# Kernel tuning notes

Measured on AMD Instinct MI355X. Metric: run time of the kernel, lower is better.

The kernel has to match this reference:

```python
import jax, jax.numpy as jnp
import numpy as np

B, N, DIM, H, DH, M = 4, 8192, 1024, 16, 64, 128
SCALE = DH ** -0.5


def setup_inputs() -> dict:
    key = jax.random.key(0)
    ks = jax.random.split(key, 8)
    x = jax.random.normal(ks[0], (B, N, DIM), jnp.float32)
    mask = jnp.ones((B, N), dtype=bool)
    W_qkv = jax.random.normal(ks[1], (DIM, 3 * H * DH), jnp.float32) * 0.02
    agent_tokens = jax.random.normal(ks[2], (H, M, DH), jnp.float32) * 0.02
    W_qa = jax.random.normal(ks[3], (H, H), jnp.float32) * 0.25
    W_ak = jax.random.normal(ks[4], (H, H), jnp.float32) * 0.25
    W_gate = jax.random.normal(ks[5], (DIM, H), jnp.float32) * 0.02
    b_gate = jnp.zeros((H,), jnp.float32)
    W_out = jax.random.normal(ks[6], (H * DH, DIM), jnp.float32) * 0.02
    return {"x": x, "mask": mask, "W_qkv": W_qkv, "agent_tokens": agent_tokens,
            "W_qa": W_qa, "W_ak": W_ak, "W_gate": W_gate, "b_gate": b_gate,
            "W_out": W_out}


def reference(x, mask, W_qkv, agent_tokens, W_qa, W_ak, W_gate, b_gate, W_out):
    b, n, dim = x.shape
    h, m, dh = agent_tokens.shape
    # qkv projection: 'b n (qkv h d) -> qkv b h n d'
    qkv = (x @ W_qkv).reshape(b, n, 3, h, dh).transpose(2, 0, 3, 1, 4)
    q, k, v = qkv[0], qkv[1], qkv[2]  # each [b,h,n,dh]
    a = agent_tokens * (dh ** -0.5)   # [h,m,dh]
    # two-hop similarities
    qa_sim = jnp.einsum('bhid,hjd->bhij', q, a)   # [b,h,n,m]
    ak_sim = jnp.einsum('hid,bhjd->bhij', a, k)   # [b,h,m,n]
    neg = -jnp.finfo(ak_sim.dtype).max
    ak_sim = jnp.where(mask[:, None, None, :], ak_sim, neg)
    qa_attn = jax.nn.softmax(qa_sim, axis=-1)
    ak_attn = jax.nn.softmax(ak_sim, axis=-1)
    # talking heads: 1x1 conv over head dim
    qa_attn = jnp.einsum('xh,bhij->bxij', W_qa, qa_attn)
    ak_attn = jnp.einsum('xh,bhij->bxij', W_ak, ak_attn)
    agent_gathered = jnp.einsum('bhmj,bhjd->bhmd', ak_attn, v)   # [b,h,m,dh]
    out = jnp.einsum('bhim,bhmd->bhid', qa_attn, agent_gathered)  # [b,h,n,dh]
    out = jnp.where(mask[:, None, :, None], out, 0.0)
    # sigmoid gate: 'b n h -> b h n 1'
    gates = jax.nn.sigmoid(jnp.einsum('bnd,dh->bnh', x, W_gate) + b_gate)
    out = out * gates.transpose(0, 2, 1)[..., None]
    # 'b h n d -> b n (h d)' then out projection
    out = out.transpose(0, 2, 1, 3).reshape(b, n, h * dh) @ W_out
    return out
```

## Files before the change

### kernel.cpp

```cpp
#include <hip/hip_runtime.h>

typedef __bf16 bf16_t;
typedef __bf16 bf16x8 __attribute__((ext_vector_type(8)));
typedef __bf16 bf16x4 __attribute__((ext_vector_type(4)));
typedef float  f32x4  __attribute__((ext_vector_type(4)));

#define B_    4
#define N_    8192
#define DIM_  1024
#define H_    16
#define DH_   64
#define M_    128
#define NT_   (B_*N_)
#define NQKV_ 3328

#define MFMA(a,b,c) __builtin_amdgcn_mfma_f32_16x16x32_bf16(a,b,c,0,0,0)

static __device__ __forceinline__ void gld_lds16(const bf16_t* g, char* l) {
  __builtin_amdgcn_global_load_lds(
      (const __attribute__((address_space(1))) unsigned int*)g,
      (__attribute__((address_space(3))) unsigned int*)l, 16, 0, 0);
}

__global__ void k_cvt(const float* __restrict__ in, bf16_t* __restrict__ out,
                      long n8) {
  long i = (long)blockIdx.x * blockDim.x + threadIdx.x;
  if (i >= n8) return;
  const float4* in4 = (const float4*)in;
  float4 f0 = in4[2*i], f1 = in4[2*i+1];
  bf16x8 o;
  o[0]=(__bf16)f0.x; o[1]=(__bf16)f0.y; o[2]=(__bf16)f0.z; o[3]=(__bf16)f0.w;
  o[4]=(__bf16)f1.x; o[5]=(__bf16)f1.y; o[6]=(__bf16)f1.z; o[7]=(__bf16)f1.w;
  ((bf16x8*)out)[i] = o;
}

__device__ __forceinline__ void tcvt_tile(const float* __restrict__ in,
                                          bf16_t* __restrict__ out,
                                          int R, int C, int bx, int by,
                                          bf16_t (*t)[33]) {
  int c0 = bx*32, r0 = by*32;
  int j = threadIdx.x & 31, i8 = threadIdx.x >> 5;
  for (int p = 0; p < 4; ++p) {
    int i = i8 + p*8, r = r0 + i, c = c0 + j;
    if (r < R && c < C) t[i][j] = (__bf16)in[(long)r*C + c];
  }
  __syncthreads();
  for (int p = 0; p < 4; ++p) {
    int i = i8 + p*8, c = c0 + i, r = r0 + j;
    if (c < C && r < R) out[(long)c*R + r] = t[j][i];
  }
}

__global__ void k_prep(const float* __restrict__ Wqkv, const float* __restrict__ Wgate,
                       const float* __restrict__ Wout, const float* __restrict__ agent,
                       bf16_t* __restrict__ WqkvT, bf16_t* __restrict__ WoutT,
                       bf16_t* __restrict__ a_s) {
  __shared__ __align__(16) bf16_t t[32][33];
  int bid = blockIdx.x;
  if (bid < 3072) {
    tcvt_tile(Wqkv, WqkvT, 1024, 3072, bid % 96, bid / 96, t);
  } else if (bid < 3104) {
    tcvt_tile(Wgate, WqkvT + (size_t)3072*DIM_, 1024, 16, 0, bid - 3072, t);
  } else if (bid < 4128) {
    int r = bid - 3104;
    tcvt_tile(Wout, WoutT, 1024, 1024, r % 32, r / 32, t);
  } else if (bid < 4192) {
    long i = (long)(bid - 4128) * 256 + threadIdx.x;
    const float4* in4 = (const float4*)agent;
    float4 f0 = in4[2*i], f1 = in4[2*i+1];
    bf16x8 o;
    o[0]=(__bf16)(f0.x*0.125f); o[1]=(__bf16)(f0.y*0.125f);
    o[2]=(__bf16)(f0.z*0.125f); o[3]=(__bf16)(f0.w*0.125f);
    o[4]=(__bf16)(f1.x*0.125f); o[5]=(__bf16)(f1.y*0.125f);
    o[6]=(__bf16)(f1.z*0.125f); o[7]=(__bf16)(f1.w*0.125f);
    ((bf16x8*)a_s)[i] = o;
  } else {
    long i = (long)(bid - 4192) * 256 + threadIdx.x;
    ((bf16x8*)(WqkvT + (size_t)3200*DIM_))[i] = (bf16x8){};
  }
}

template<int MODE>
__global__ __launch_bounds__(512, 2)
void k_g256(const bf16_t* __restrict__ A, const bf16_t* __restrict__ Bt,
            void* __restrict__ Cout, bf16_t* __restrict__ k2out,
            bf16_t* __restrict__ vTout,
            const float* __restrict__ bg, float* __restrict__ gates,
            int Ndim, int Kdim) {
  __shared__ __align__(16) char lds[131072];
  const int tid = threadIdx.x;
  const int wid = tid >> 6, lane = tid & 63;
  const int g = lane >> 4, r15 = lane & 15;
  const int wr = wid >> 2, wc = wid & 3;
  const int nbx = gridDim.x;
  const int flat = blockIdx.y * nbx + blockIdx.x;
  const int q8 = (nbx * gridDim.y) >> 3;
  const int swz = (flat & 7) * q8 + (flat >> 3);
  const long m0 = (long)(swz / nbx) * 256, n0 = (long)(swz % nbx) * 256;

  f32x4 acc[8][4] = {};
  const int ITERS = Kdim >> 7;

  auto stg = [&](const bf16_t* Gp, long grow0, int tile, int ab, int half) {
    char* base = lds + (((tile & 1)*2 + ab)*2 + half)*16384;
    long kb = (long)tile * 64;
    #pragma unroll
    for (int j = 0; j < 2; ++j) {
      int o = tid*16 + j*8192;
      int row = o >> 7;
      int c16 = ((o >> 4) & 7) ^ (row & 7);
      const bf16_t* src = Gp + (grow0 + half*128 + row)*Kdim + kb + c16*8;
      gld_lds16(src, base + (tid & ~63)*16 + j*8192);
    }
  };
  auto aread = [&](int buf, int q, bf16x8 af[2][2]) {
    const char* base = lds + ((buf*2 + 0)*2 + wr)*16384;
    #pragma unroll
    for (int ml = 0; ml < 2; ++ml) {
      int rl = q*32 + ml*16 + r15;
      #pragma unroll
      for (int kk = 0; kk < 2; ++kk)
        af[ml][kk] = *(const bf16x8*)(base + rl*128 + ((kk*64 + g*16) ^ ((rl & 7) << 4)));
    }
  };
  auto bread = [&](int buf, bf16x8 bf[4][2]) {
    const char* base = lds + ((buf*2 + 1)*2 + (wc >> 1))*16384;
    #pragma unroll
    for (int ni = 0; ni < 4; ++ni) {
      int rl = (wc & 1)*64 + ni*16 + r15;
      #pragma unroll
      for (int kk = 0; kk < 2; ++kk)
        bf[ni][kk] = *(const bf16x8*)(base + rl*128 + ((kk*64 + g*16) ^ ((rl & 7) << 4)));
    }
  };

  stg(A, m0, 0, 0, 0); stg(A, m0, 0, 0, 1);
  stg(Bt, n0, 0, 1, 0); stg(Bt, n0, 0, 1, 1);
  stg(Bt, n0, 1, 1, 0); stg(Bt, n0, 1, 1, 1);

  for (int it = 0; it < ITERS; ++it) {
    const int t0 = 2*it, t1 = 2*it + 1;
    const bool more = (it < ITERS - 1);
    bf16x8 bf[4][2], af[2][2];

#define PH_MFMA(q)                                                        \
    __builtin_amdgcn_s_setprio(1);                                        \
    _Pragma("unroll")                                                     \
    for (int ml = 0; ml < 2; ++ml)                                        \
      _Pragma("unroll")                                                   \
      for (int ni = 0; ni < 4; ++ni)                                      \
        _Pragma("unroll")                                                 \
        for (int kk = 0; kk < 2; ++kk)                                    \
          acc[(q)*2+ml][ni] = MFMA(af[ml][kk], bf[ni][kk], acc[(q)*2+ml][ni]); \
    __builtin_amdgcn_s_setprio(0);
#define BAR asm volatile("s_barrier" ::: "memory")

    stg(A, m0, t1, 0, 0);
    asm volatile("s_waitcnt vmcnt(4)" ::: "memory");
    BAR;
    bread(0, bf); aread(0, 0, af);
    PH_MFMA(0); BAR;
    aread(0, 1, af);
    stg(A, m0, t1, 0, 1);
    BAR; PH_MFMA(1); BAR;
    aread(0, 2, af);
    if (more) stg(Bt, n0, t0 + 2, 1, 0);
    BAR; PH_MFMA(2); BAR;
    aread(0, 3, af);
    if (more) stg(Bt, n0, t0 + 2, 1, 1);
    BAR; PH_MFMA(3); BAR;
    if (more) {
      stg(A, m0, t0 + 2, 0, 0);
      asm volatile("s_waitcnt vmcnt(4)" ::: "memory");
    } else {
      asm volatile("s_waitcnt vmcnt(0)" ::: "memory");
    }
    BAR;
    bread(1, bf); aread(1, 0, af);
    PH_MFMA(0); BAR;
    aread(1, 1, af);
    if (more) stg(A, m0, t0 + 2, 0, 1);
    BAR; PH_MFMA(1); BAR;
    aread(1, 2, af);
    if (more) stg(Bt, n0, t1 + 2, 1, 0);
    BAR; PH_MFMA(2); BAR;
    aread(1, 3, af);
    if (more) stg(Bt, n0, t1 + 2, 1, 1);
    BAR; PH_MFMA(3); BAR;
#undef PH_MFMA
#undef BAR
  }

  if (MODE == 1 && n0 >= 3072) {
    if (wc == 0) {
      float bgv = bg[r15];
      #pragma unroll
      for (int mi = 0; mi < 8; ++mi)
        #pragma unroll
        for (int r = 0; r < 4; ++r) {
          long tok = m0 + wr*128 + mi*16 + g*4 + r;
          float v = acc[mi][0][r] + bgv;
          gates[tok*16 + r15] = 1.0f / (1.0f + __expf(-v));
        }
    }
  } else if (MODE == 1 && n0 >= 2048) {
    long bidx = m0 >> 13;
    long nbase = (m0 & (N_-1)) + wr*128 + g*4;
    #pragma unroll
    for (int mi = 0; mi < 8; ++mi)
      #pragma unroll
      for (int ni = 0; ni < 4; ++ni) {
        long c = (n0 - 2048) + wc*64 + ni*16 + r15;
        bf16x4 o;
        #pragma unroll
        for (int r = 0; r < 4; ++r) o[r] = (__bf16)acc[mi][ni][r];
        *(bf16x4*)(vTout + (bidx*DIM_ + c)*N_ + nbase + mi*16) = o;
      }
  } else if (MODE == 1 && n0 >= 1024) {
    int h = (int)((n0 - 1024 + wc*64) >> 6);
    #pragma unroll
    for (int mi = 0; mi < 8; ++mi)
      #pragma unroll
      for (int ni = 0; ni < 4; ++ni) {
        int dh = ni*16 + r15;
        #pragma unroll
        for (int r = 0; r < 4; ++r) {
          long row = m0 + wr*128 + mi*16 + g*4 + r;
          long bidx = row >> 13, nb = row & (N_-1);
          k2out[((bidx*H_ + h)*N_ + nb)*DH_ + dh] = (__bf16)acc[mi][ni][r];
        }
      }
  } else if (MODE == 1) {
    bf16_t* q = (bf16_t*)Cout;
    #pragma unroll
    for (int mi = 0; mi < 8; ++mi)
      #pragma unroll
      for (int ni = 0; ni < 4; ++ni)
        #pragma unroll
        for (int r = 0; r < 4; ++r) {
          long row = m0 + wr*128 + mi*16 + g*4 + r;
          long col = n0 + wc*64 + ni*16 + r15;
          q[row * DIM_ + col] = (__bf16)acc[mi][ni][r];
        }
  } else {
    float* C = (float*)Cout;
    #pragma unroll
    for (int mi = 0; mi < 8; ++mi)
      #pragma unroll
      for (int ni = 0; ni < 4; ++ni)
        #pragma unroll
        for (int r = 0; r < 4; ++r) {
          long row = m0 + wr*128 + mi*16 + g*4 + r;
          long col = n0 + wc*64 + ni*16 + r15;
          C[row * Ndim + col] = acc[mi][ni][r];
        }
  }
}

__global__ __launch_bounds__(256)
void k_stats(const bf16_t* __restrict__ k2, const bf16_t* __restrict__ a_s,
             float* __restrict__ statp) {
  int ch = blockIdx.x, h = blockIdx.y, b = blockIdx.z;
  int wave = threadIdx.x >> 6, lane = threadIdx.x & 63;
  int g = lane >> 4, r15 = lane & 15;
  bf16x8 af[2][2];
  #pragma unroll
  for (int mi = 0; mi < 2; ++mi)
    #pragma unroll
    for (int ks = 0; ks < 2; ++ks)
      af[mi][ks] = *(const bf16x8*)(a_s + (h*M_ + wave*32 + mi*16 + r15)*DH_ + ks*32 + g*8);
  float rsum[2][4] = {};
  long nbase = (long)ch * 1024;
  const bf16_t* kb = k2 + ((long)(b*H_ + h)*N_)*DH_;
  for (int ns = 0; ns < 64; ++ns) {
    long n = nbase + ns*16;
    const bf16_t* kp = kb + (n + r15)*DH_;
    bf16x8 bf0 = *(const bf16x8*)(kp + g*8);
    bf16x8 bf1 = *(const bf16x8*)(kp + 32 + g*8);
    #pragma unroll
    for (int mi = 0; mi < 2; ++mi) {
      f32x4 acc = {};
      acc = MFMA(af[mi][0], bf0, acc);
      acc = MFMA(af[mi][1], bf1, acc);
      #pragma unroll
      for (int r = 0; r < 4; ++r) rsum[mi][r] += __expf(acc[r]);
    }
  }
  #pragma unroll
  for (int mi = 0; mi < 2; ++mi)
    #pragma unroll
    for (int r = 0; r < 4; ++r) {
      float s = rsum[mi][r];
      s += __shfl_xor(s,1); s += __shfl_xor(s,2);
      s += __shfl_xor(s,4); s += __shfl_xor(s,8);
      if (r15 == 0) {
        int m = wave*32 + mi*16 + g*4 + r;
        statp[((((long)b*H_ + h)*8 + ch))*M_ + m] = s;
      }
    }
}

__global__ __launch_bounds__(256)
void k_akmix(const bf16_t* __restrict__ k2, const bf16_t* __restrict__ a_s,
             const float* __restrict__ statp, const float* __restrict__ Wak,
             bf16_t* __restrict__ mixP) {
  __shared__ __align__(16) char P[32*32*16*2];
  __shared__ float SL[16][128];
  __shared__ float WL[256];
  int tid = threadIdx.x;
  int wave = tid >> 6, lane = tid & 63, g = lane >> 4, r15 = lane & 15;
  int b = blockIdx.y;
  long nt0 = (long)blockIdx.x * 32;
  WL[tid] = Wak[tid];
  for (int i = tid; i < 2048; i += 256) {
    int h = i >> 7, m = i & 127;
    float D = 0.f;
    #pragma unroll
    for (int c = 0; c < 8; ++c) D += statp[(((long)b*H_ + h)*8 + c)*M_ + m];
    SL[h][m] = 1.0f / D;
  }
  __syncthreads();

  for (int mc = 0; mc < 4; ++mc) {
    for (int hi = 0; hi < 4; ++hi) {
      int h = wave*4 + hi;
      bf16x8 af[2][2], bfr[2][2];
      #pragma unroll
      for (int mi = 0; mi < 2; ++mi)
        #pragma unroll
        for (int ks = 0; ks < 2; ++ks)
          af[mi][ks] = *(const bf16x8*)(a_s + (h*M_ + mc*32 + mi*16 + r15)*DH_ + ks*32 + g*8);
      #pragma unroll
      for (int nj = 0; nj < 2; ++nj) {
        const bf16_t* kp = k2 + ((long)(b*H_ + h)*N_ + nt0 + nj*16 + r15)*DH_;
        bfr[nj][0] = *(const bf16x8*)(kp + g*8);
        bfr[nj][1] = *(const bf16x8*)(kp + 32 + g*8);
      }
      #pragma unroll
      for (int mi = 0; mi < 2; ++mi)
        #pragma unroll
        for (int nj = 0; nj < 2; ++nj) {
          f32x4 acc = {};
          acc = MFMA(af[mi][0], bfr[nj][0], acc);
          acc = MFMA(af[mi][1], bfr[nj][1], acc);
          #pragma unroll
          for (int r = 0; r < 4; ++r) {
            int m = mi*16 + g*4 + r;
            float p = __expf(acc[r]) * SL[h][mc*32 + m];
            int n = nj*16 + r15;
            int byteoff = ((h*1024 + m*32 + n)*2) ^ ((m & 7) << 4);
            *(bf16_t*)(P + byteoff) = (__bf16)p;
          }
        }
    }
    __syncthreads();

    {
      int m = lane >> 1, nh = lane & 1;
      int swzb = (m & 7) << 4;
      float accv[4][16] = {};
      for (int h = 0; h < 16; ++h) {
        int base = h*2048 + m*64 + nh*32;
        bf16x8 p0 = *(const bf16x8*)(P + ((base)    ^ swzb));
        bf16x8 p1 = *(const bf16x8*)(P + ((base+16) ^ swzb));
        float pf[16];
        #pragma unroll
        for (int j = 0; j < 8; ++j) { pf[j] = (float)p0[j]; pf[8+j] = (float)p1[j]; }
        #pragma unroll
        for (int xi = 0; xi < 4; ++xi) {
          float w = WL[(wave*4 + xi)*16 + h];
          #pragma unroll
          for (int n = 0; n < 16; ++n) accv[xi][n] += w * pf[n];
        }
      }
      #pragma unroll
      for (int xi = 0; xi < 4; ++xi) {
        int x = wave*4 + xi;
        bf16x8 o0, o1;
        #pragma unroll
        for (int j = 0; j < 8; ++j) {
          o0[j] = (__bf16)accv[xi][j];
          o1[j] = (__bf16)accv[xi][8+j];
        }
        bf16_t* dst = mixP + (((long)b*H_ + x)*M_ + mc*32 + m)*N_ + nt0 + nh*16;
        *(bf16x8*)dst = o0;
        *(bf16x8*)(dst + 8) = o1;
      }
    }
    __syncthreads();
  }
}

__global__ __launch_bounds__(256)
void k_G(const bf16_t* __restrict__ mixP, const bf16_t* __restrict__ vT,
         float* __restrict__ Gpart) {
  int kc = blockIdx.x, x = blockIdx.y, b = blockIdx.z;
  int wave = threadIdx.x >> 6, lane = threadIdx.x & 63;
  int g = lane >> 4, r15 = lane & 15;
  f32x4 acc[2][4] = {};
  long nb = (long)kc * 1024;
  for (int ns = 0; ns < 32; ++ns) {
    long n = nb + ns*32;
    bf16x8 af[2], bfv[4];
    #pragma unroll
    for (int mi = 0; mi < 2; ++mi)
      af[mi] = *(const bf16x8*)(mixP + (((long)b*H_ + x)*M_ + wave*32 + mi*16 + r15)*N_ + n + g*8);
    #pragma unroll
    for (int di = 0; di < 4; ++di)
      bfv[di] = *(const bf16x8*)(vT + ((long)b*DIM_ + x*64 + di*16 + r15)*N_ + n + g*8);
    #pragma unroll
    for (int mi = 0; mi < 2; ++mi)
      #pragma unroll
      for (int di = 0; di < 4; ++di)
        acc[mi][di] = MFMA(af[mi], bfv[di], acc[mi][di]);
  }
  #pragma unroll
  for (int mi = 0; mi < 2; ++mi)
    #pragma unroll
    for (int di = 0; di < 4; ++di)
      #pragma unroll
      for (int r = 0; r < 4; ++r) {
        int m = wave*32 + mi*16 + g*4 + r;
        Gpart[((((long)b*8 + kc)*H_ + x)*M_ + m)*DH_ + di*16 + r15] = acc[mi][di][r];
      }
}

__global__ void k_Gc(const float* __restrict__ Gpart, bf16_t* __restrict__ GT) {
  long idx = (long)blockIdx.x*256 + threadIdx.x;
  if (idx >= (long)B_*H_*DH_*M_) return;
  int m = (int)(idx & 127);
  int d = (int)((idx >> 7) & 63);
  int x = (int)((idx >> 13) & 15);
  int b = (int)(idx >> 17);
  float s = 0.f;
  #pragma unroll
  for (int kc = 0; kc < 8; ++kc)
    s += Gpart[((((long)b*8 + kc)*H_ + x)*M_ + m)*DH_ + d];
  GT[(((long)b*H_ + x)*DH_ + d)*M_ + m] = (__bf16)s;
}

__global__ __launch_bounds__(256)
void k_qa_out(const bf16_t* __restrict__ q, const bf16_t* __restrict__ a_s,
              const float* __restrict__ Wqa, const bf16_t* __restrict__ GT,
              const float* __restrict__ gates, bf16_t* __restrict__ attn_out) {
  __shared__ __align__(16) char P[16*16*128*2];
  __shared__ float W[256];
  int b = blockIdx.y;
  long t0 = (long)blockIdx.x * 16;
  int wave = threadIdx.x >> 6, lane = threadIdx.x & 63;
  int g = lane >> 4, r15 = lane & 15;
  W[threadIdx.x] = Wqa[threadIdx.x];

  for (int hi = 0; hi < 4; ++hi) {
    int h = wave*4 + hi;
    const bf16_t* qp = q + ((long)b*N_ + t0 + r15)*DIM_ + h*64;
    bf16x8 aq0 = *(const bf16x8*)(qp + g*8);
    bf16x8 aq1 = *(const bf16x8*)(qp + 32 + g*8);
    f32x4 acc8[8];
    #pragma unroll
    for (int ni = 0; ni < 8; ++ni) {
      const bf16_t* ap = a_s + (h*M_ + ni*16 + r15)*DH_;
      bf16x8 b0 = *(const bf16x8*)(ap + g*8);
      bf16x8 b1 = *(const bf16x8*)(ap + 32 + g*8);
      f32x4 t = {};
      t = MFMA(aq0, b0, t); t = MFMA(aq1, b1, t);
      acc8[ni] = t;
    }
    #pragma unroll
    for (int r = 0; r < 4; ++r) {
      float e[8]; float s = 0.f;
      #pragma unroll
      for (int ni = 0; ni < 8; ++ni) { e[ni] = __expf(acc8[ni][r]); s += e[ni]; }
      s += __shfl_xor(s,1); s += __shfl_xor(s,2); s += __shfl_xor(s,4); s += __shfl_xor(s,8);
      float invs = 1.0f/s;
      int tok = g*4 + r;
      #pragma unroll
      for (int ni = 0; ni < 8; ++ni) {
        int byteoff = (((h*16 + tok)*128 + ni*16 + r15)*2) ^ ((tok&7)<<4);
        *(bf16_t*)(P + byteoff) = (__bf16)(e[ni]*invs);
      }
    }
  }
  __syncthreads();

  for (int xi = 0; xi < 4; ++xi) {
    int x = wave*4 + xi;
    float macc[4][8] = {};
    for (int h = 0; h < 16; ++h) {
      float wv = W[x*16 + h];
      #pragma unroll
      for (int ks = 0; ks < 4; ++ks) {
        int byteoff = (((h*16 + r15)*128 + ks*32 + g*8)*2) ^ ((r15&7)<<4);
        bf16x8 p = *(const bf16x8*)(P + byteoff);
        #pragma unroll
        for (int j = 0; j < 8; ++j) macc[ks][j] += wv * (float)p[j];
      }
    }
    bf16x8 av[4];
    #pragma unroll
    for (int ks = 0; ks < 4; ++ks)
      #pragma unroll
      for (int j = 0; j < 8; ++j) av[ks][j] = (__bf16)macc[ks][j];
    f32x4 oacc[4] = {};
    #pragma unroll
    for (int di = 0; di < 4; ++di)
      #pragma unroll
      for (int ks = 0; ks < 4; ++ks) {
        bf16x8 bv = *(const bf16x8*)(GT + (((long)b*H_ + x)*DH_ + di*16 + r15)*M_ + ks*32 + g*8);
        oacc[di] = MFMA(av[ks], bv, oacc[di]);
      }
    #pragma unroll
    for (int di = 0; di < 4; ++di)
      #pragma unroll
      for (int r = 0; r < 4; ++r) {
        int tok = g*4 + r;
        float gv = gates[((long)b*N_ + t0 + tok)*16 + x];
        attn_out[((long)b*N_ + t0 + tok)*DIM_ + x*64 + di*16 + r15] = (__bf16)(oacc[di][r]*gv);
      }
  }
}

extern "C" void kernel_launch(void* const* d_in, const int* in_sizes, int n_in,
                              void* d_out, int out_size, void* d_ws, size_t ws_size,
                              hipStream_t stream) {
  const float* x      = (const float*)d_in[0];
  const float* W_qkv  = (const float*)d_in[2];
  const float* agent  = (const float*)d_in[3];
  const float* W_qa   = (const float*)d_in[4];
  const float* W_ak   = (const float*)d_in[5];
  const float* W_gate = (const float*)d_in[6];
  const float* b_gate = (const float*)d_in[7];
  const float* W_out  = (const float*)d_in[8];
  float* out = (float*)d_out;

  char* ws = (char*)d_ws;
  size_t off = 0;
  auto alloc = [&](size_t bytes) {
    char* p = ws + off; off += (bytes + 255) & ~(size_t)255; return p;
  };
  bf16_t* q     = (bf16_t*)alloc((size_t)NT_*DIM_*2);
  bf16_t* k2    = (bf16_t*)alloc((size_t)NT_*DIM_*2);
  bf16_t* xbf   = (bf16_t*)alloc((size_t)NT_*DIM_*2);
  bf16_t* vT    = (bf16_t*)alloc((size_t)B_*DIM_*N_*2);
  bf16_t* mixP  = (bf16_t*)alloc((size_t)B_*H_*M_*N_*2);
  bf16_t* WqkvT = (bf16_t*)alloc((size_t)NQKV_*DIM_*2);
  bf16_t* WoutT = (bf16_t*)alloc((size_t)DIM_*DIM_*2);
  bf16_t* a_s   = (bf16_t*)alloc((size_t)H_*M_*DH_*2);
  float*  statp = (float*)alloc((size_t)B_*H_*8*M_*4);
  float*  gates = (float*)alloc((size_t)NT_*H_*4);
  float*  Gpart = (float*)alloc((size_t)B_*8*H_*M_*DH_*4);
  bf16_t* GT    = (bf16_t*)alloc((size_t)B_*H_*DH_*M_*2);
  bf16_t* attn  = xbf;
  (void)ws_size; (void)in_sizes; (void)n_in; (void)out_size;

  k_prep<<<4256, 256, 0, stream>>>(W_qkv, W_gate, W_out, agent, WqkvT, WoutT, a_s);
  k_cvt<<<(int)((long)NT_*DIM_/8/256), 256, 0, stream>>>(x, xbf, (long)NT_*DIM_/8);

  k_g256<1><<<dim3(NQKV_/256, NT_/256), 512, 0, stream>>>(
      xbf, WqkvT, q, k2, vT, b_gate, gates, DIM_, DIM_);

  k_stats<<<dim3(8, H_, B_), 256, 0, stream>>>(k2, a_s, statp);
  k_akmix<<<dim3(N_/32, B_), 256, 0, stream>>>(k2, a_s, statp, W_ak, mixP);
  k_G<<<dim3(8, H_, B_), 256, 0, stream>>>(mixP, vT, Gpart);
  k_Gc<<<(B_*H_*DH_*M_ + 255)/256, 256, 0, stream>>>(Gpart, GT);

  k_qa_out<<<dim3(N_/16, B_), 256, 0, stream>>>(q, a_s, W_qa, GT, gates, attn);
  k_g256<0><<<dim3(DIM_/256, NT_/256), 512, 0, stream>>>(
      attn, WoutT, out, nullptr, nullptr, nullptr, nullptr, DIM_, DIM_);
}
```

Measured before the change: 740.6 us.

## Fuse agent-key softmax mixing with value gather and merge x conversion into prep

Merges the k_akmix and k_G kernels into a single k_akpv kernel. The head-mixed attention probabilities stay in LDS and feed MFMAs against vT directly, so the 256MB mixP buffer is never written to or read back from global memory. The x fp32→bf16 conversion also moves into the k_prep launch, which removes one kernel launch. In exchange the grid is smaller (256 blocks), each block loops sequentially over 32 token steps with two syncthreads per step, and k2 is recomputed once per m-chunk (8 times instead of 4).

```diff
diff --git a/kernel.cpp b/kernel.cpp
--- a/kernel.cpp
+++ b/kernel.cpp
@@ -20,18 +20,6 @@
   __builtin_amdgcn_global_load_lds(
       (const __attribute__((address_space(1))) unsigned int*)g,
       (__attribute__((address_space(3))) unsigned int*)l, 16, 0, 0);
-}
-
-__global__ void k_cvt(const float* __restrict__ in, bf16_t* __restrict__ out,
-                      long n8) {
-  long i = (long)blockIdx.x * blockDim.x + threadIdx.x;
-  if (i >= n8) return;
-  const float4* in4 = (const float4*)in;
-  float4 f0 = in4[2*i], f1 = in4[2*i+1];
-  bf16x8 o;
-  o[0]=(__bf16)f0.x; o[1]=(__bf16)f0.y; o[2]=(__bf16)f0.z; o[3]=(__bf16)f0.w;
-  o[4]=(__bf16)f1.x; o[5]=(__bf16)f1.y; o[6]=(__bf16)f1.z; o[7]=(__bf16)f1.w;
-  ((bf16x8*)out)[i] = o;
 }
 
 __device__ __forceinline__ void tcvt_tile(const float* __restrict__ in,
@@ -53,8 +41,9 @@
 
 __global__ void k_prep(const float* __restrict__ Wqkv, const float* __restrict__ Wgate,
                        const float* __restrict__ Wout, const float* __restrict__ agent,
+                       const float* __restrict__ x,
                        bf16_t* __restrict__ WqkvT, bf16_t* __restrict__ WoutT,
-                       bf16_t* __restrict__ a_s) {
+                       bf16_t* __restrict__ a_s, bf16_t* __restrict__ xbf) {
   __shared__ __align__(16) bf16_t t[32][33];
   int bid = blockIdx.x;
   if (bid < 3072) {
@@ -74,9 +63,17 @@
     o[4]=(__bf16)(f1.x*0.125f); o[5]=(__bf16)(f1.y*0.125f);
     o[6]=(__bf16)(f1.z*0.125f); o[7]=(__bf16)(f1.w*0.125f);
     ((bf16x8*)a_s)[i] = o;
-  } else {
+  } else if (bid < 4256) {
     long i = (long)(bid - 4192) * 256 + threadIdx.x;
     ((bf16x8*)(WqkvT + (size_t)3200*DIM_))[i] = (bf16x8){};
+  } else {
+    long i = (long)(bid - 4256) * 256 + threadIdx.x;
+    const float4* in4 = (const float4*)x;
+    float4 f0 = in4[2*i], f1 = in4[2*i+1];
+    bf16x8 o;
+    o[0]=(__bf16)f0.x; o[1]=(__bf16)f0.y; o[2]=(__bf16)f0.z; o[3]=(__bf16)f0.w;
+    o[4]=(__bf16)f1.x; o[5]=(__bf16)f1.y; o[6]=(__bf16)f1.z; o[7]=(__bf16)f1.w;
+    ((bf16x8*)xbf)[i] = o;
   }
 }
 
@@ -300,129 +297,97 @@
     }
 }
 
-__global__ __launch_bounds__(256)
-void k_akmix(const bf16_t* __restrict__ k2, const bf16_t* __restrict__ a_s,
-             const float* __restrict__ statp, const float* __restrict__ Wak,
-             bf16_t* __restrict__ mixP) {
-  __shared__ __align__(16) char P[32*32*16*2];
-  __shared__ float SL[16][128];
+__global__ __launch_bounds__(256, 2)
+void k_akpv(const bf16_t* __restrict__ k2, const bf16_t* __restrict__ a_s,
+            const float* __restrict__ statp, const float* __restrict__ Wak,
+            const bf16_t* __restrict__ vT, float* __restrict__ Gpart) {
+  __shared__ __align__(16) char P[16*16*32*2];
+  __shared__ float SL[16][16];
   __shared__ float WL[256];
   int tid = threadIdx.x;
   int wave = tid >> 6, lane = tid & 63, g = lane >> 4, r15 = lane & 15;
-  int b = blockIdx.y;
-  long nt0 = (long)blockIdx.x * 32;
+  int nc = blockIdx.x, mc = blockIdx.y, b = blockIdx.z;
   WL[tid] = Wak[tid];
-  for (int i = tid; i < 2048; i += 256) {
-    int h = i >> 7, m = i & 127;
+  {
+    int h = tid >> 4, m = tid & 15;
     float D = 0.f;
     #pragma unroll
-    for (int c = 0; c < 8; ++c) D += statp[(((long)b*H_ + h)*8 + c)*M_ + m];
+    for (int c = 0; c < 8; ++c)
+      D += statp[(((long)b*H_ + h)*8 + c)*M_ + mc*16 + m];
     SL[h][m] = 1.0f / D;
   }
   __syncthreads();
 
-  for (int mc = 0; mc < 4; ++mc) {
+  f32x4 acc[4][4] = {};
+  for (int ts = 0; ts < 32; ++ts) {
+    long nt0 = (long)nc*1024 + ts*32;
     for (int hi = 0; hi < 4; ++hi) {
       int h = wave*4 + hi;
-      bf16x8 af[2][2], bfr[2][2];
-      #pragma unroll
-      for (int mi = 0; mi < 2; ++mi)
-        #pragma unroll
-        for (int ks = 0; ks < 2; ++ks)
-          af[mi][ks] = *(const bf16x8*)(a_s + (h*M_ + mc*32 + mi*16 + r15)*DH_ + ks*32 + g*8);
+      const bf16_t* ap = a_s + (h*M_ + mc*16 + r15)*DH_;
+      bf16x8 af0 = *(const bf16x8*)(ap + g*8);
+      bf16x8 af1 = *(const bf16x8*)(ap + 32 + g*8);
       #pragma unroll
       for (int nj = 0; nj < 2; ++nj) {
         const bf16_t* kp = k2 + ((long)(b*H_ + h)*N_ + nt0 + nj*16 + r15)*DH_;
-        bfr[nj][0] = *(const bf16x8*)(kp + g*8);
-        bfr[nj][1] = *(const bf16x8*)(kp + 32 + g*8);
-      }
-      #pragma unroll
-      for (int mi = 0; mi < 2; ++mi)
-        #pragma unroll
-        for (int nj = 0; nj < 2; ++nj) {
-          f32x4 acc = {};
-          acc = MFMA(af[mi][0], bfr[nj][0], acc);
-          acc = MFMA(af[mi][1], bfr[nj][1], acc);
-          #pragma unroll
-          for (int r = 0; r < 4; ++r) {
-            int m = mi*16 + g*4 + r;
-            float p = __expf(acc[r]) * SL[h][mc*32 + m];
-            int n = nj*16 + r15;
-            int byteoff = ((h*1024 + m*32 + n)*2) ^ ((m & 7) << 4);
-            *(bf16_t*)(P + byteoff) = (__bf16)p;
-          }
-        }
+        bf16x8 b0 = *(const bf16x8*)(kp + g*8);
+        bf16x8 b1 = *(const bf16x8*)(kp + 32 + g*8);
+        f32x4 s = {};
+        s = MFMA(af0, b0, s);
+        s = MFMA(af1, b1, s);
+        #pragma unroll
+        for (int r = 0; r < 4; ++r) {
+          int m = g*4 + r;
+          float p = __expf(s[r]) * SL[h][m];
+          int n = nj*16 + r15;
+          int byteoff = ((h*512 + m*32 + n)*2) ^ ((m & 7) << 4);
+          *(bf16_t*)(P + byteoff) = (__bf16)p;
+        }
+      }
     }
     __syncthreads();
 
     {
-      int m = lane >> 1, nh = lane & 1;
-      int swzb = (m & 7) << 4;
-      float accv[4][16] = {};
+      float accv[4][8] = {};
+      int sw = (r15 & 7) << 4;
       for (int h = 0; h < 16; ++h) {
-        int base = h*2048 + m*64 + nh*32;
-        bf16x8 p0 = *(const bf16x8*)(P + ((base)    ^ swzb));
-        bf16x8 p1 = *(const bf16x8*)(P + ((base+16) ^ swzb));
-        float pf[16];
-        #pragma unroll
-        for (int j = 0; j < 8; ++j) { pf[j] = (float)p0[j]; pf[8+j] = (float)p1[j]; }
+        bf16x8 pr = *(const bf16x8*)(P + (((h*512 + r15*32 + g*8)*2) ^ sw));
+        float pf[8];
+        #pragma unroll
+        for (int j = 0; j < 8; ++j) pf[j] = (float)pr[j];
         #pragma unroll
         for (int xi = 0; xi < 4; ++xi) {
           float w = WL[(wave*4 + xi)*16 + h];
           #pragma unroll
-          for (int n = 0; n < 16; ++n) accv[xi][n] += w * pf[n];
+          for (int j = 0; j < 8; ++j) accv[xi][j] += w * pf[j];
         }
       }
       #pragma unroll
       for (int xi = 0; xi < 4; ++xi) {
         int x = wave*4 + xi;
-        bf16x8 o0, o1;
-        #pragma unroll
-        for (int j = 0; j < 8; ++j) {
-          o0[j] = (__bf16)accv[xi][j];
-          o1[j] = (__bf16)accv[xi][8+j];
-        }
-        bf16_t* dst = mixP + (((long)b*H_ + x)*M_ + mc*32 + m)*N_ + nt0 + nh*16;
-        *(bf16x8*)dst = o0;
-        *(bf16x8*)(dst + 8) = o1;
+        bf16x8 av;
+        #pragma unroll
+        for (int j = 0; j < 8; ++j) av[j] = (__bf16)accv[xi][j];
+        #pragma unroll
+        for (int di = 0; di < 4; ++di) {
+          bf16x8 bv = *(const bf16x8*)(vT + ((long)b*DIM_ + x*64 + di*16 + r15)*N_ + nt0 + g*8);
+          acc[xi][di] = MFMA(av, bv, acc[xi][di]);
+        }
       }
     }
     __syncthreads();
   }
-}
-
-__global__ __launch_bounds__(256)
-void k_G(const bf16_t* __restrict__ mixP, const bf16_t* __restrict__ vT,
-         float* __restrict__ Gpart) {
-  int kc = blockIdx.x, x = blockIdx.y, b = blockIdx.z;
-  int wave = threadIdx.x >> 6, lane = threadIdx.x & 63;
-  int g = lane >> 4, r15 = lane & 15;
-  f32x4 acc[2][4] = {};
-  long nb = (long)kc * 1024;
-  for (int ns = 0; ns < 32; ++ns) {
-    long n = nb + ns*32;
-    bf16x8 af[2], bfv[4];
-    #pragma unroll
-    for (int mi = 0; mi < 2; ++mi)
-      af[mi] = *(const bf16x8*)(mixP + (((long)b*H_ + x)*M_ + wave*32 + mi*16 + r15)*N_ + n + g*8);
+
+  #pragma unroll
+  for (int xi = 0; xi < 4; ++xi) {
+    int x = wave*4 + xi;
     #pragma unroll
     for (int di = 0; di < 4; ++di)
-      bfv[di] = *(const bf16x8*)(vT + ((long)b*DIM_ + x*64 + di*16 + r15)*N_ + n + g*8);
-    #pragma unroll
-    for (int mi = 0; mi < 2; ++mi)
-      #pragma unroll
-      for (int di = 0; di < 4; ++di)
-        acc[mi][di] = MFMA(af[mi], bfv[di], acc[mi][di]);
-  }
-  #pragma unroll
-  for (int mi = 0; mi < 2; ++mi)
-    #pragma unroll
-    for (int di = 0; di < 4; ++di)
       #pragma unroll
       for (int r = 0; r < 4; ++r) {
-        int m = wave*32 + mi*16 + g*4 + r;
-        Gpart[((((long)b*8 + kc)*H_ + x)*M_ + m)*DH_ + di*16 + r15] = acc[mi][di][r];
-      }
+        int m = mc*16 + g*4 + r;
+        Gpart[((((long)b*8 + nc)*H_ + x)*M_ + m)*DH_ + di*16 + r15] = acc[xi][di][r];
+      }
+  }
 }
 
 __global__ void k_Gc(const float* __restrict__ Gpart, bf16_t* __restrict__ GT) {
@@ -434,8 +399,8 @@
   int b = (int)(idx >> 17);
   float s = 0.f;
   #pragma unroll
-  for (int kc = 0; kc < 8; ++kc)
-    s += Gpart[((((long)b*8 + kc)*H_ + x)*M_ + m)*DH_ + d];
+  for (int nc = 0; nc < 8; ++nc)
+    s += Gpart[((((long)b*8 + nc)*H_ + x)*M_ + m)*DH_ + d];
   GT[(((long)b*H_ + x)*DH_ + d)*M_ + m] = (__bf16)s;
 }
 
@@ -542,7 +507,6 @@
   bf16_t* k2    = (bf16_t*)alloc((size_t)NT_*DIM_*2);
   bf16_t* xbf   = (bf16_t*)alloc((size_t)NT_*DIM_*2);
   bf16_t* vT    = (bf16_t*)alloc((size_t)B_*DIM_*N_*2);
-  bf16_t* mixP  = (bf16_t*)alloc((size_t)B_*H_*M_*N_*2);
   bf16_t* WqkvT = (bf16_t*)alloc((size_t)NQKV_*DIM_*2);
   bf16_t* WoutT = (bf16_t*)alloc((size_t)DIM_*DIM_*2);
   bf16_t* a_s   = (bf16_t*)alloc((size_t)H_*M_*DH_*2);
@@ -553,15 +517,14 @@
   bf16_t* attn  = xbf;
   (void)ws_size; (void)in_sizes; (void)n_in; (void)out_size;
 
-  k_prep<<<4256, 256, 0, stream>>>(W_qkv, W_gate, W_out, agent, WqkvT, WoutT, a_s);
-  k_cvt<<<(int)((long)NT_*DIM_/8/256), 256, 0, stream>>>(x, xbf, (long)NT_*DIM_/8);
+  k_prep<<<4256 + 16384, 256, 0, stream>>>(
+      W_qkv, W_gate, W_out, agent, x, WqkvT, WoutT, a_s, xbf);
 
   k_g256<1><<<dim3(NQKV_/256, NT_/256), 512, 0, stream>>>(
       xbf, WqkvT, q, k2, vT, b_gate, gates, DIM_, DIM_);
 
   k_stats<<<dim3(8, H_, B_), 256, 0, stream>>>(k2, a_s, statp);
-  k_akmix<<<dim3(N_/32, B_), 256, 0, stream>>>(k2, a_s, statp, W_ak, mixP);
-  k_G<<<dim3(8, H_, B_), 256, 0, stream>>>(mixP, vT, Gpart);
+  k_akpv<<<dim3(8, 8, B_), 256, 0, stream>>>(k2, a_s, statp, W_ak, vT, Gpart);
   k_Gc<<<(B_*H_*DH_*M_ + 255)/256, 256, 0, stream>>>(Gpart, GT);
 
   k_qa_out<<<dim3(N_/16, B_), 256, 0, stream>>>(q, a_s, W_qa, GT, gates, attn);
```

Measured after the change: 986.6 us. +33.2%, slower.
